# Kernel tuning notes

Measured on AMD Instinct MI355X. Metric: run time of the kernel, lower is better.

The kernel has to match this reference:

```python
import jax, jax.numpy as jnp
import numpy as np
import math

V, D, H, NL, L, B = 32000, 1024, 16, 6, 1024, 2
HD = D // H
EPS = 1e-5


def _positional(L, D):
    # matches torch: exp(arange(0,D,2) * -(log(1000)/D))
    div = jnp.exp(jnp.arange(0, D, 2, dtype=jnp.float32) * (-math.log(1000.0) / D))
    k = jnp.arange(L, dtype=jnp.float32)[:, None]
    pos = jnp.zeros((L, D), dtype=jnp.float32)
    pos = pos.at[:, 0::2].set(jnp.sin(k * div))
    pos = pos.at[:, 1::2].set(jnp.cos(k * div))
    return pos[None]  # [1, L, D]


def setup_inputs() -> dict:
    key = jax.random.key(0)
    ks = jax.random.split(key, 12)
    s = 0.02
    tokens = jax.random.randint(ks[0], (B, L), 0, V)
    emb = jax.random.normal(ks[1], (V, D), jnp.float32) * s
    pos = _positional(L, D)
    ln1_g = jnp.ones((NL, D), jnp.float32)
    ln1_b = jnp.zeros((NL, D), jnp.float32)
    ln2_g = jnp.ones((NL, D), jnp.float32)
    ln2_b = jnp.zeros((NL, D), jnp.float32)
    attn_w = jax.random.normal(ks[2], (NL, D, 3 * D), jnp.float32) * s
    attn_b = jnp.zeros((NL, 3 * D), jnp.float32)
    proj_w = jax.random.normal(ks[3], (NL, D, D), jnp.float32) * s
    proj_b = jnp.zeros((NL, D), jnp.float32)
    mlp_w1 = jax.random.normal(ks[4], (NL, D, 4 * D), jnp.float32) * s
    mlp_b1 = jnp.zeros((NL, 4 * D), jnp.float32)
    mlp_w2 = jax.random.normal(ks[5], (NL, 4 * D, D), jnp.float32) * s
    mlp_b2 = jnp.zeros((NL, D), jnp.float32)
    out_w = jax.random.normal(ks[6], (D, V), jnp.float32) * s
    return dict(tokens=tokens, pos=pos, emb=emb,
                ln1_g=ln1_g, ln1_b=ln1_b, ln2_g=ln2_g, ln2_b=ln2_b,
                attn_w=attn_w, attn_b=attn_b, proj_w=proj_w, proj_b=proj_b,
                mlp_w1=mlp_w1, mlp_b1=mlp_b1, mlp_w2=mlp_w2, mlp_b2=mlp_b2,
                out_w=out_w)


def _ln(x, g, b):
    mu = jnp.mean(x, -1, keepdims=True)
    var = jnp.mean(jnp.square(x - mu), -1, keepdims=True)
    return (x - mu) * jax.lax.rsqrt(var + EPS) * g + b


def _block(x, p, causal_mask):
    ln1_g, ln1_b, ln2_g, ln2_b, aw, ab, pw, pb, w1, b1, w2, b2 = p
    h = _ln(x, ln1_g, ln1_b)
    qkv = h @ aw + ab                      # [B, L, 3D]
    q, k, v = jnp.split(qkv, 3, axis=-1)
    Bc, Lc = x.shape[0], x.shape[1]
    q = q.reshape(Bc, Lc, H, HD)
    k = k.reshape(Bc, Lc, H, HD)
    v = v.reshape(Bc, Lc, H, HD)
    scores = jnp.einsum('blhd,bmhd->bhlm', q, k) * (1.0 / math.sqrt(HD))
    scores = jnp.where(causal_mask, scores, -jnp.inf)
    attn = jax.nn.softmax(scores, axis=-1)
    y = jnp.einsum('bhlm,bmhd->blhd', attn, v).reshape(Bc, Lc, D)
    x = x + (y @ pw + pb)
    r = _ln(x, ln2_g, ln2_b)
    # NOTE: original ModuleList order applies GELU AFTER the second linear
    r = jax.nn.gelu((r @ w1 + b1) @ w2 + b2, approximate=False)
    return x + r


def reference(tokens, pos, emb, ln1_g, ln1_b, ln2_g, ln2_b,
              attn_w, attn_b, proj_w, proj_b,
              mlp_w1, mlp_b1, mlp_w2, mlp_b2, out_w):
    x = emb[tokens] + pos                  # [B, L, D]
    Lc = x.shape[1]
    causal_mask = jnp.tril(jnp.ones((Lc, Lc), bool))[None, None]
    for i in range(NL):
        p = (ln1_g[i], ln1_b[i], ln2_g[i], ln2_b[i],
             attn_w[i], attn_b[i], proj_w[i], proj_b[i],
             mlp_w1[i], mlp_b1[i], mlp_w2[i], mlp_b2[i])
        x = _block(x, p, causal_mask)
    return x @ out_w                       # [B, L, V] logits
```

## Files before the change

kernel.cpp:

```cpp
#include <hip/hip_runtime.h>
#include <hip/hip_bf16.h>
#include <math.h>

typedef __bf16 bf16;
typedef __bf16 bf16x4 __attribute__((ext_vector_type(4)));
typedef __bf16 bf16x8 __attribute__((ext_vector_type(8)));
typedef float f32x4 __attribute__((ext_vector_type(4)));

__device__ __forceinline__ void gld_lds16(const void* g, void* l) {
    __builtin_amdgcn_global_load_lds(
        (const __attribute__((address_space(1))) unsigned int*)g,
        (__attribute__((address_space(3))) unsigned int*)l, 16, 0, 0);
}

#define VMW(n) asm volatile("s_waitcnt vmcnt(" #n ")" ::: "memory")
#define BARR() asm volatile("s_barrier" ::: "memory")

__global__ __launch_bounds__(256) void k_embed(const int* __restrict__ tok,
                                               const float* __restrict__ emb,
                                               const float* __restrict__ pos,
                                               float* __restrict__ x) {
    int row = blockIdx.x;
    int l = row & 1023;
    int tk = tok[row];
    const float4* e = (const float4*)(emb + (size_t)tk * 1024);
    const float4* p = (const float4*)(pos + (size_t)l * 1024);
    float4* o = (float4*)(x + (size_t)row * 1024);
    float4 a = e[threadIdx.x], b = p[threadIdx.x];
    o[threadIdx.x] = make_float4(a.x + b.x, a.y + b.y, a.z + b.z, a.w + b.w);
}

__global__ __launch_bounds__(256) void k_ln(const float* __restrict__ x,
                                            const float* __restrict__ g,
                                            const float* __restrict__ b,
                                            bf16* __restrict__ out) {
    int row = blockIdx.x;
    int t = threadIdx.x;
    const float4* xr = (const float4*)(x + (size_t)row * 1024);
    float4 v = xr[t];
    float s1 = v.x + v.y + v.z + v.w;
    float s2 = v.x * v.x + v.y * v.y + v.z * v.z + v.w * v.w;
#pragma unroll
    for (int o = 32; o; o >>= 1) { s1 += __shfl_down(s1, o); s2 += __shfl_down(s2, o); }
    __shared__ float ps1[4], ps2[4], stat[2];
    int lane = t & 63, wid = t >> 6;
    if (lane == 0) { ps1[wid] = s1; ps2[wid] = s2; }
    __syncthreads();
    if (t == 0) {
        float a1 = ps1[0] + ps1[1] + ps1[2] + ps1[3];
        float a2 = ps2[0] + ps2[1] + ps2[2] + ps2[3];
        float mu = a1 * (1.f / 1024.f);
        float var = a2 * (1.f / 1024.f) - mu * mu;
        stat[0] = mu; stat[1] = rsqrtf(var + 1e-5f);
    }
    __syncthreads();
    float mu = stat[0], rs = stat[1];
    const float4* gv = (const float4*)g;
    const float4* bv = (const float4*)b;
    float4 gg = gv[t], bb = bv[t];
    bf16x4 o4;
    o4[0] = (bf16)((v.x - mu) * rs * gg.x + bb.x);
    o4[1] = (bf16)((v.y - mu) * rs * gg.y + bb.y);
    o4[2] = (bf16)((v.z - mu) * rs * gg.z + bb.z);
    o4[3] = (bf16)((v.w - mu) * rs * gg.w + bb.w);
    *(bf16x4*)(out + (size_t)row * 1024 + t * 4) = o4;
}

__global__ __launch_bounds__(256) void k_cast(const float* __restrict__ x, bf16* __restrict__ o) {
    int i = blockIdx.x * 256 + threadIdx.x;
    float4 v = ((const float4*)x)[i];
    bf16x4 b;
    b[0] = (bf16)v.x; b[1] = (bf16)v.y; b[2] = (bf16)v.z; b[3] = (bf16)v.w;
    ((bf16x4*)o)[i] = b;
}

__device__ __forceinline__ void transpose64(const float* __restrict__ W,
                                            bf16* __restrict__ WT,
                                            int K, int N, int n0, int k0, int t,
                                            float (*tile)[65]) {
    int tx = t & 15, ty = t >> 4;
#pragma unroll
    for (int i = 0; i < 64; i += 16) {
        float4 v = *(const float4*)&W[(size_t)(k0 + ty + i) * N + n0 + tx * 4];
        tile[ty + i][tx * 4 + 0] = v.x;
        tile[ty + i][tx * 4 + 1] = v.y;
        tile[ty + i][tx * 4 + 2] = v.z;
        tile[ty + i][tx * 4 + 3] = v.w;
    }
    __syncthreads();
    int n = t >> 3, ks = t & 7;
#pragma unroll
    for (int pass = 0; pass < 2; ++pass) {
        int nn = n + pass * 32;
        bf16x8 v;
#pragma unroll
        for (int j = 0; j < 8; ++j) v[j] = (bf16)tile[ks * 8 + j][nn];
        *(bf16x8*)&WT[(size_t)(n0 + nn) * K + k0 + ks * 8] = v;
    }
}

__global__ __launch_bounds__(256) void k_transpose_layer(const float* __restrict__ aw,
                                                         const float* __restrict__ pw,
                                                         const float* __restrict__ m1,
                                                         const float* __restrict__ m2,
                                                         bf16* __restrict__ wT) {
    __shared__ float tile[64][65];
    int bid = blockIdx.x;
    const float* src; bf16* dst; int K, N, tn, tk;
    if (bid < 768)       { src = aw; dst = wT;            K = 1024; N = 3072; tn = bid % 48; tk = bid / 48; }
    else if (bid < 1024) { int b = bid - 768;  src = pw; dst = wT + 3145728; K = 1024; N = 1024; tn = b % 16; tk = b / 16; }
    else if (bid < 2048) { int b = bid - 1024; src = m1; dst = wT + 4194304; K = 1024; N = 4096; tn = b % 64; tk = b / 64; }
    else                 { int b = bid - 2048; src = m2; dst = wT + 8388608; K = 4096; N = 1024; tn = b % 16; tk = b / 16; }
    transpose64(src, dst, K, N, tn * 64, tk * 64, threadIdx.x, tile);
}

__global__ __launch_bounds__(256) void k_transpose_out(const float* __restrict__ W,
                                                       bf16* __restrict__ WT) {
    __shared__ float tile[64][65];
    int bid = blockIdx.x;
    int tn = bid % 500, tk = bid / 500;
    transpose64(W, WT, 1024, 32000, tn * 64, tk * 64, threadIdx.x, tile);
}

__device__ __forceinline__ void stage128(const char* Ab, const char* Bb,
                                         char* As, char* Bs, int Kb, int k0b, int t) {
#pragma unroll
    for (int j = 0; j < 4; ++j) {
        int idx = j * 256 + t;
        int row = idx >> 3;
        int cb = (idx & 7) << 4;
        int scb = cb ^ ((row & 7) << 4);
        gld_lds16(Ab + (size_t)row * Kb + k0b + scb, As + idx * 16);
        gld_lds16(Bb + (size_t)row * Kb + k0b + scb, Bs + idx * 16);
    }
}

template <int EPI>
__global__ __launch_bounds__(256) void k_gemm2(const bf16* __restrict__ A,
                                               const bf16* __restrict__ BT,
                                               const float* __restrict__ bias,
                                               const float* __restrict__ resid,
                                               float* __restrict__ outf,
                                               bf16* __restrict__ outb,
                                               int N, int K) {
    __shared__ __align__(16) bf16 As[2][128 * 64];
    __shared__ __align__(16) bf16 Bs[2][128 * 64];
    int per = gridDim.x >> 3;
    int tile = (blockIdx.x & 7) * per + (blockIdx.x >> 3);
    int bm = tile & 15, bn = tile >> 4;
    int t = threadIdx.x, lane = t & 63;
    int wr = t >> 7, wc = (t >> 6) & 1;
    f32x4 acc[4][4] = {};
    const char* Ab = (const char*)(A + (size_t)bm * 128 * K);
    const char* Bb = (const char*)(BT + (size_t)bn * 128 * K);
    int Kb = K * 2;
    int nk = K >> 6;
    stage128(Ab, Bb, (char*)As[0], (char*)Bs[0], Kb, 0, t);
    VMW(0); BARR();
    for (int tt = 0; tt < nk; ++tt) {
        int cur = tt & 1;
        if (tt + 1 < nk)
            stage128(Ab, Bb, (char*)As[cur ^ 1], (char*)Bs[cur ^ 1], Kb, (tt + 1) * 128, t);
        const char* Ac = (const char*)As[cur];
        const char* Bc = (const char*)Bs[cur];
#pragma unroll
        for (int kk = 0; kk < 2; ++kk) {
            bf16x8 af[4], bfr[4];
            int cb = kk * 64 + ((lane >> 4) << 4);
#pragma unroll
            for (int m = 0; m < 4; ++m) {
                int r = wr * 64 + m * 16 + (lane & 15);
                af[m] = *(const bf16x8*)(Ac + r * 128 + (cb ^ ((r & 7) << 4)));
            }
#pragma unroll
            for (int n = 0; n < 4; ++n) {
                int r = wc * 64 + n * 16 + (lane & 15);
                bfr[n] = *(const bf16x8*)(Bc + r * 128 + (cb ^ ((r & 7) << 4)));
            }
#pragma unroll
            for (int m = 0; m < 4; ++m)
#pragma unroll
                for (int n = 0; n < 4; ++n)
                    acc[m][n] = __builtin_amdgcn_mfma_f32_16x16x32_bf16(af[m], bfr[n], acc[m][n], 0, 0, 0);
        }
        VMW(0); BARR();
    }
    int row0 = bm * 128 + wr * 64 + ((lane >> 4) << 2);
    int col0 = bn * 128 + wc * 64 + (lane & 15);
#pragma unroll
    for (int m = 0; m < 4; ++m) {
#pragma unroll
        for (int n = 0; n < 4; ++n) {
            int col = col0 + n * 16;
            float bv = bias[col];
#pragma unroll
            for (int r = 0; r < 4; ++r) {
                int row = row0 + m * 16 + r;
                size_t idx = (size_t)row * N + col;
                float v = acc[m][n][r] + bv;
                if (EPI == 0) {
                    outb[idx] = (bf16)v;
                } else if (EPI == 1) {
                    outf[idx] = resid[idx] + v;
                } else {
                    outf[idx] = resid[idx] + 0.5f * v * (1.0f + erff(v * 0.70710678118f));
                }
            }
        }
    }
}

__device__ __forceinline__ void stage64(const char* Ab, const char* Bb,
                                        char* As, char* Bs, int Kb, int k0b, int t) {
#pragma unroll
    for (int j = 0; j < 2; ++j) {
        int idx = j * 256 + t;
        int row = idx >> 3;
        int cb = (idx & 7) << 4;
        int scb = cb ^ ((row & 7) << 4);
        gld_lds16(Ab + (size_t)row * Kb + k0b + scb, As + idx * 16);
        gld_lds16(Bb + (size_t)row * Kb + k0b + scb, Bs + idx * 16);
    }
}

template <int EPI>
__global__ __launch_bounds__(256) void k_gemm64(const bf16* __restrict__ A,
                                                const bf16* __restrict__ BT,
                                                const float* __restrict__ bias,
                                                const float* __restrict__ resid,
                                                float* __restrict__ outf,
                                                int N, int K) {
    __shared__ __align__(16) bf16 As[2][64 * 64];
    __shared__ __align__(16) bf16 Bs[2][64 * 64];
    int per = gridDim.x >> 3;
    int tile = (blockIdx.x & 7) * per + (blockIdx.x >> 3);
    int bm = tile & 31, bn = tile >> 5;
    int t = threadIdx.x, lane = t & 63, wid = t >> 6;
    f32x4 acc[4] = {};
    const char* Ab = (const char*)(A + (size_t)bm * 64 * K);
    const char* Bb = (const char*)(BT + (size_t)bn * 64 * K);
    int Kb = K * 2;
    int nk = K >> 6;
    stage64(Ab, Bb, (char*)As[0], (char*)Bs[0], Kb, 0, t);
    VMW(0); BARR();
    for (int tt = 0; tt < nk; ++tt) {
        int cur = tt & 1;
        if (tt + 1 < nk)
            stage64(Ab, Bb, (char*)As[cur ^ 1], (char*)Bs[cur ^ 1], Kb, (tt + 1) * 128, t);
        const char* Ac = (const char*)As[cur];
        const char* Bc = (const char*)Bs[cur];
#pragma unroll
        for (int kk = 0; kk < 2; ++kk) {
            int cb = kk * 64 + ((lane >> 4) << 4);
            int ra = wid * 16 + (lane & 15);
            bf16x8 af = *(const bf16x8*)(Ac + ra * 128 + (cb ^ ((ra & 7) << 4)));
            bf16x8 bfr[4];
#pragma unroll
            for (int n = 0; n < 4; ++n) {
                int r = n * 16 + (lane & 15);
                bfr[n] = *(const bf16x8*)(Bc + r * 128 + (cb ^ ((r & 7) << 4)));
            }
#pragma unroll
            for (int n = 0; n < 4; ++n)
                acc[n] = __builtin_amdgcn_mfma_f32_16x16x32_bf16(af, bfr[n], acc[n], 0, 0, 0);
        }
        VMW(0); BARR();
    }
    int row0 = bm * 64 + wid * 16 + ((lane >> 4) << 2);
    int col0 = bn * 64 + (lane & 15);
#pragma unroll
    for (int n = 0; n < 4; ++n) {
        int col = col0 + n * 16;
        float bv = bias[col];
#pragma unroll
        for (int r = 0; r < 4; ++r) {
            int row = row0 + r;
            size_t idx = (size_t)row * N + col;
            float v = acc[n][r] + bv;
            if (EPI == 1) {
                outf[idx] = resid[idx] + v;
            } else {
                outf[idx] = resid[idx] + 0.5f * v * (1.0f + erff(v * 0.70710678118f));
            }
        }
    }
}

__device__ __forceinline__ void stage_full256(const char* gtile, char* ldst,
                                              int Kb, int t) {
#pragma unroll
    for (int j = 0; j < 4; ++j) {
        int idx = j * 512 + t;
        int row = idx >> 3;
        int cb = (idx & 7) << 4;
        int scb = cb ^ ((row & 7) << 4);
        gld_lds16(gtile + (size_t)row * Kb + scb, ldst + idx * 16);
    }
}

__device__ __forceinline__ void stage_half256(const char* gtile, char* ldst,
                                              int Kb, int t, int half) {
#pragma unroll
    for (int j = 0; j < 2; ++j) {
        int idx = (half * 2 + j) * 512 + t;
        int row = idx >> 3;
        int cb = (idx & 7) << 4;
        int scb = cb ^ ((row & 7) << 4);
        gld_lds16(gtile + (size_t)row * Kb + scb, ldst + idx * 16);
    }
}

template <int MH, int NH>
__device__ __forceinline__ void phase_rd(const char* Ac, const char* Bc,
                                         int lrow, int lk, int wm, int wn,
                                         bf16x8 (&af)[4][2], bf16x8 (&bfr)[2][2]) {
#pragma unroll
    for (int kk = 0; kk < 2; ++kk) {
        int cb = kk * 64 + lk * 16;
#pragma unroll
        for (int m = 0; m < 4; ++m) {
            int row = (MH * 4 + m) * 32 + wm * 16 + lrow;
            af[m][kk] = *(const bf16x8*)(Ac + row * 128 + (cb ^ ((row & 7) << 4)));
        }
#pragma unroll
        for (int n = 0; n < 2; ++n) {
            int row = (NH * 2 + n) * 64 + wn * 16 + lrow;
            bfr[n][kk] = *(const bf16x8*)(Bc + row * 128 + (cb ^ ((row & 7) << 4)));
        }
    }
}

template <int MH, int NH>
__device__ __forceinline__ void phase_mm(bf16x8 (&af)[4][2], bf16x8 (&bfr)[2][2],
                                         f32x4 (&acc)[8][4]) {
    __builtin_amdgcn_s_setprio(1);
#pragma unroll
    for (int kk = 0; kk < 2; ++kk)
#pragma unroll
        for (int m = 0; m < 4; ++m)
#pragma unroll
            for (int n = 0; n < 2; ++n)
                acc[MH * 4 + m][NH * 2 + n] = __builtin_amdgcn_mfma_f32_16x16x32_bf16(
                    af[m][kk], bfr[n][kk], acc[MH * 4 + m][NH * 2 + n], 0, 0, 0);
    __builtin_amdgcn_s_setprio(0);
    __builtin_amdgcn_sched_barrier(0);
}

__global__ __launch_bounds__(512, 1) void k_gemm256(const bf16* __restrict__ A,
                                                    const bf16* __restrict__ BT,
                                                    float* __restrict__ outf,
                                                    int N, int K) {
    __shared__ __align__(16) bf16 Asb[2][256 * 64];
    __shared__ __align__(16) bf16 Bsb[3][256 * 64];
    int t = threadIdx.x, lane = t & 63, wid = t >> 6;
    int wm = wid >> 2, wn = wid & 3;
    int lrow = lane & 15, lk = lane >> 4;
    int tile = (blockIdx.x & 7) * 125 + (blockIdx.x >> 3);
    int bm = tile & 7;
    int bn = tile >> 3;

    const char* Ab = (const char*)(A + (size_t)bm * 256 * K);
    const char* Bb = (const char*)(BT + (size_t)bn * 256 * K);
    int Kb = K * 2;
    int nk = K >> 6;
    f32x4 acc[8][4] = {};

    stage_full256(Ab, (char*)Asb[0], Kb, t);
    stage_full256(Bb, (char*)Bsb[0], Kb, t);
    stage_full256(Bb + 128, (char*)Bsb[1], Kb, t);

    for (int tt = 0; tt < nk; ++tt) {
        int ka = (tt + 1 < nk) ? tt + 1 : nk - 1;
        int kb = (tt + 2 < nk) ? tt + 2 : nk - 1;
        const char* Ac = (const char*)Asb[tt & 1];
        const char* Bc = (const char*)Bsb[tt % 3];
        char* An = (char*)Asb[(tt + 1) & 1];
        char* Bn = (char*)Bsb[(tt + 2) % 3];
        const char* Ag = Ab + (size_t)ka * 128;
        const char* Bg = Bb + (size_t)kb * 128;
        VMW(4); BARR();
        bf16x8 af[4][2], bfr[2][2];
        phase_rd<0, 0>(Ac, Bc, lrow, lk, wm, wn, af, bfr);
        stage_half256(Ag, An, Kb, t, 0);
        BARR();
        phase_mm<0, 0>(af, bfr, acc);
        BARR();
        phase_rd<0, 1>(Ac, Bc, lrow, lk, wm, wn, af, bfr);
        stage_half256(Ag, An, Kb, t, 1);
        BARR();
        phase_mm<0, 1>(af, bfr, acc);
        BARR();
        phase_rd<1, 0>(Ac, Bc, lrow, lk, wm, wn, af, bfr);
        stage_half256(Bg, Bn, Kb, t, 0);
        BARR();
        phase_mm<1, 0>(af, bfr, acc);
        BARR();
        phase_rd<1, 1>(Ac, Bc, lrow, lk, wm, wn, af, bfr);
        stage_half256(Bg, Bn, Kb, t, 1);
        BARR();
        phase_mm<1, 1>(af, bfr, acc);
        BARR();
    }

    size_t row0 = (size_t)bm * 256 + wm * 16 + (lane >> 4) * 4;
    int col0 = bn * 256 + wn * 16 + (lane & 15);
#pragma unroll
    for (int mi = 0; mi < 8; ++mi) {
#pragma unroll
        for (int ni = 0; ni < 4; ++ni) {
            int col = col0 + ni * 64;
#pragma unroll
            for (int r = 0; r < 4; ++r) {
                size_t row = row0 + mi * 32 + r;
                outf[row * N + col] = acc[mi][ni][r];
            }
        }
    }
}

__global__ __launch_bounds__(256) void k_attn(const bf16* __restrict__ qkv, bf16* __restrict__ y) {
    int tile = (blockIdx.x & 7) * 64 + (blockIdx.x >> 3);
    int qb = tile & 15;
    int bh = tile >> 4;
    int b = bh >> 4, h = bh & 15;
    int t = threadIdx.x, lane = t & 63, wid = t >> 6;
    int lr = lane & 15, lk = lane >> 4;
    int tok0 = b << 10;
    int q0 = qb << 6;
    __shared__ __align__(16) bf16 Qs[64 * 64];
    __shared__ __align__(16) bf16 Ks[64 * 64];
    __shared__ __align__(16) bf16 Vt[64 * 64];
    __shared__ __align__(16) bf16 Ps[4 * 16 * 64];
    const char* qbase = (const char*)qkv;
#pragma unroll
    for (int j = 0; j < 2; ++j) {
        int off = (j * 256 + t) * 16;
        int row = off >> 7, colb = off & 127;
        int scb = colb ^ ((row & 7) << 4);
        gld_lds16(qbase + ((size_t)(tok0 + q0 + row) * 3072 + h * 64) * 2 + scb, (char*)Qs + off);
    }
    VMW(0);
    __syncthreads();
    int qrw = wid * 16 + lr;
    int qsw = (qrw & 7) << 4;
    bf16x8 aq0 = *(const bf16x8*)((const char*)Qs + qrw * 128 + ((lk * 16) ^ qsw));
    bf16x8 aq1 = *(const bf16x8*)((const char*)Qs + qrw * 128 + ((64 + lk * 16) ^ qsw));
    f32x4 o[4] = {};
    float mrun[4], lrun[4];
#pragma unroll
    for (int r = 0; r < 4; ++r) { mrun[r] = -INFINITY; lrun[r] = 0.f; }
    int qrow = q0 + wid * 16 + lk * 4;

    for (int kv0 = 0; kv0 <= q0; kv0 += 64) {
        __syncthreads();
#pragma unroll
        for (int j = 0; j < 2; ++j) {
            int off = (j * 256 + t) * 16;
            int row = off >> 7, colb = off & 127;
            int scb = colb ^ ((row & 7) << 4);
            gld_lds16(qbase + ((size_t)(tok0 + kv0 + row) * 3072 + 1024 + h * 64) * 2 + scb,
                      (char*)Ks + off);
        }
        {
            int kv = t >> 2, d0 = (t & 3) * 16;
            const bf16* vrow = qkv + (size_t)(tok0 + kv0 + kv) * 3072 + 2048 + h * 64 + d0;
#pragma unroll
            for (int e4 = 0; e4 < 4; ++e4) {
                bf16x4 vv = *(const bf16x4*)(vrow + e4 * 4);
#pragma unroll
                for (int i = 0; i < 4; ++i) {
                    int d = d0 + e4 * 4 + i;
                    Vt[d * 64 + (kv ^ ((d & 7) << 3))] = vv[i];
                }
            }
        }
        VMW(0);
        __syncthreads();
        f32x4 s[4];
#pragma unroll
        for (int n = 0; n < 4; ++n) {
            int krw = n * 16 + lr;
            int ksw = (krw & 7) << 4;
            const char* kb = (const char*)Ks + krw * 128;
            bf16x8 bk0 = *(const bf16x8*)(kb + ((lk * 16) ^ ksw));
            bf16x8 bk1 = *(const bf16x8*)(kb + ((64 + lk * 16) ^ ksw));
            f32x4 z = {};
            z = __builtin_amdgcn_mfma_f32_16x16x32_bf16(aq0, bk0, z, 0, 0, 0);
            z = __builtin_amdgcn_mfma_f32_16x16x32_bf16(aq1, bk1, z, 0, 0, 0);
            s[n] = z;
        }
        float mx[4];
#pragma unroll
        for (int r = 0; r < 4; ++r) mx[r] = -INFINITY;
#pragma unroll
        for (int n = 0; n < 4; ++n) {
            int col = kv0 + n * 16 + lr;
#pragma unroll
            for (int r = 0; r < 4; ++r) {
                float sv = s[n][r] * 0.125f;
                sv = (col <= qrow + r) ? sv : -INFINITY;
                s[n][r] = sv;
                mx[r] = fmaxf(mx[r], sv);
            }
        }
#pragma unroll
        for (int r = 0; r < 4; ++r)
#pragma unroll
            for (int m = 1; m < 16; m <<= 1) mx[r] = fmaxf(mx[r], __shfl_xor(mx[r], m));
        float scl[4];
#pragma unroll
        for (int r = 0; r < 4; ++r) {
            float mn = fmaxf(mrun[r], mx[r]);
            scl[r] = __expf(mrun[r] - mn);
            mrun[r] = mn;
        }
        float rs[4] = {0.f, 0.f, 0.f, 0.f};
#pragma unroll
        for (int n = 0; n < 4; ++n)
#pragma unroll
            for (int r = 0; r < 4; ++r) {
                float p = __expf(s[n][r] - mrun[r]);
                s[n][r] = p;
                rs[r] += p;
            }
#pragma unroll
        for (int r = 0; r < 4; ++r) {
#pragma unroll
            for (int m = 1; m < 16; m <<= 1) rs[r] += __shfl_xor(rs[r], m);
            lrun[r] = lrun[r] * scl[r] + rs[r];
        }
#pragma unroll
        for (int n = 0; n < 4; ++n)
#pragma unroll
            for (int r = 0; r < 4; ++r) {
                o[n][r] *= scl[r];
                int prow = lk * 4 + r;
                Ps[wid * 1024 + prow * 64 + ((n * 16 + lr) ^ ((prow & 7) << 3))] = (bf16)s[n][r];
            }
        int psw = (lr & 7) << 3;
        const bf16* pb = Ps + wid * 1024 + lr * 64;
        bf16x8 ap0 = *(const bf16x8*)(pb + ((lk * 8) ^ psw));
        bf16x8 ap1 = *(const bf16x8*)(pb + ((32 + lk * 8) ^ psw));
#pragma unroll
        for (int n = 0; n < 4; ++n) {
            int vrw = n * 16 + lr;
            int vsw = (vrw & 7) << 3;
            const bf16* vb = Vt + vrw * 64;
            bf16x8 bv0 = *(const bf16x8*)(vb + ((lk * 8) ^ vsw));
            bf16x8 bv1 = *(const bf16x8*)(vb + ((32 + lk * 8) ^ vsw));
            o[n] = __builtin_amdgcn_mfma_f32_16x16x32_bf16(ap0, bv0, o[n], 0, 0, 0);
            o[n] = __builtin_amdgcn_mfma_f32_16x16x32_bf16(ap1, bv1, o[n], 0, 0, 0);
        }
    }
#pragma unroll
    for (int n = 0; n < 4; ++n)
#pragma unroll
        for (int r = 0; r < 4; ++r) {
            int row = tok0 + qrow + r;
            y[(size_t)row * 1024 + h * 64 + n * 16 + lr] = (bf16)(o[n][r] / lrun[r]);
        }
}

extern "C" void kernel_launch(void* const* d_in, const int* in_sizes, int n_in,
                              void* d_out, int out_size, void* d_ws, size_t ws_size,
                              hipStream_t stream) {
    const int*   tokens = (const int*)d_in[0];
    const float* pos    = (const float*)d_in[1];
    const float* emb    = (const float*)d_in[2];
    const float* ln1_g  = (const float*)d_in[3];
    const float* ln1_b  = (const float*)d_in[4];
    const float* ln2_g  = (const float*)d_in[5];
    const float* ln2_b  = (const float*)d_in[6];
    const float* attn_w = (const float*)d_in[7];
    const float* attn_b = (const float*)d_in[8];
    const float* proj_w = (const float*)d_in[9];
    const float* proj_b = (const float*)d_in[10];
    const float* mlp_w1 = (const float*)d_in[11];
    const float* mlp_b1 = (const float*)d_in[12];
    const float* mlp_w2 = (const float*)d_in[13];
    const float* mlp_b2 = (const float*)d_in[14];
    const float* out_w  = (const float*)d_in[15];
    float* out = (float*)d_out;

    char* ws = (char*)d_ws;
    size_t off = 0;
    auto alloc = [&](size_t bytes) {
        void* p = ws + off;
        off = (off + bytes + 255) & ~(size_t)255;
        return p;
    };
    float* x   = (float*)alloc((size_t)2048 * 1024 * 4);
    bf16* hb   = (bf16*)alloc((size_t)2048 * 1024 * 2);
    bf16* qkvb = (bf16*)alloc((size_t)2048 * 3072 * 2);
    bf16* yb   = (bf16*)alloc((size_t)2048 * 1024 * 2);
    bf16* hidb = (bf16*)alloc((size_t)2048 * 4096 * 2);
    bf16* wT   = (bf16*)alloc((size_t)32000 * 1024 * 2);

    k_embed<<<2048, 256, 0, stream>>>(tokens, emb, pos, x);

    for (int i = 0; i < 6; ++i) {
        k_transpose_layer<<<3072, 256, 0, stream>>>(
            attn_w + (size_t)i * 1024 * 3072, proj_w + (size_t)i * 1024 * 1024,
            mlp_w1 + (size_t)i * 1024 * 4096, mlp_w2 + (size_t)i * 4096 * 1024, wT);
        k_ln<<<2048, 256, 0, stream>>>(x, ln1_g + i * 1024, ln1_b + i * 1024, hb);
        k_gemm2<0><<<384, 256, 0, stream>>>(hb, wT, attn_b + i * 3072,
                                            nullptr, nullptr, qkvb, 3072, 1024);
        k_attn<<<512, 256, 0, stream>>>(qkvb, yb);
        k_gemm64<1><<<512, 256, 0, stream>>>(yb, wT + 3145728, proj_b + i * 1024,
                                             x, x, 1024, 1024);
        k_ln<<<2048, 256, 0, stream>>>(x, ln2_g + i * 1024, ln2_b + i * 1024, hb);
        k_gemm2<0><<<512, 256, 0, stream>>>(hb, wT + 4194304, mlp_b1 + i * 4096,
                                            nullptr, nullptr, hidb, 4096, 1024);
        k_gemm64<2><<<512, 256, 0, stream>>>(hidb, wT + 8388608, mlp_b2 + i * 1024,
                                             x, x, 1024, 4096);
    }

    k_cast<<<2048, 256, 0, stream>>>(x, hb);
    k_transpose_out<<<8000, 256, 0, stream>>>(out_w, wT);
    k_gemm256<<<1000, 512, 0, stream>>>(hb, wT, out, 32000, 1024);
}
```

Before: 1.217 ms.

## Overlap next-layer weight transposes with attention and fuse final bf16 cast

```diff
diff --git a/kernel.cpp b/kernel.cpp
--- a/kernel.cpp
+++ b/kernel.cpp
@@ -66,14 +66,6 @@
     *(bf16x4*)(out + (size_t)row * 1024 + t * 4) = o4;
 }
 
-__global__ __launch_bounds__(256) void k_cast(const float* __restrict__ x, bf16* __restrict__ o) {
-    int i = blockIdx.x * 256 + threadIdx.x;
-    float4 v = ((const float4*)x)[i];
-    bf16x4 b;
-    b[0] = (bf16)v.x; b[1] = (bf16)v.y; b[2] = (bf16)v.z; b[3] = (bf16)v.w;
-    ((bf16x4*)o)[i] = b;
-}
-
 __device__ __forceinline__ void transpose64(const float* __restrict__ W,
                                             bf16* __restrict__ WT,
                                             int K, int N, int n0, int k0, int t,
@@ -99,27 +91,25 @@
     }
 }
 
+__device__ __forceinline__ void tr_layer_block(int bid,
+                                               const float* aw, const float* pw,
+                                               const float* m1, const float* m2,
+                                               bf16* wT, int t, float (*tile)[65]) {
+    const float* src; bf16* dst; int K, N, tn, tk;
+    if (bid < 768)       { src = aw; dst = wT;            K = 1024; N = 3072; tn = bid % 48; tk = bid / 48; }
+    else if (bid < 1024) { int b = bid - 768;  src = pw; dst = wT + 3145728; K = 1024; N = 1024; tn = b % 16; tk = b / 16; }
+    else if (bid < 2048) { int b = bid - 1024; src = m1; dst = wT + 4194304; K = 1024; N = 4096; tn = b % 64; tk = b / 64; }
+    else                 { int b = bid - 2048; src = m2; dst = wT + 8388608; K = 4096; N = 1024; tn = b % 16; tk = b / 16; }
+    transpose64(src, dst, K, N, tn * 64, tk * 64, t, tile);
+}
+
 __global__ __launch_bounds__(256) void k_transpose_layer(const float* __restrict__ aw,
                                                          const float* __restrict__ pw,
                                                          const float* __restrict__ m1,
                                                          const float* __restrict__ m2,
                                                          bf16* __restrict__ wT) {
     __shared__ float tile[64][65];
-    int bid = blockIdx.x;
-    const float* src; bf16* dst; int K, N, tn, tk;
-    if (bid < 768)       { src = aw; dst = wT;            K = 1024; N = 3072; tn = bid % 48; tk = bid / 48; }
-    else if (bid < 1024) { int b = bid - 768;  src = pw; dst = wT + 3145728; K = 1024; N = 1024; tn = b % 16; tk = b / 16; }
-    else if (bid < 2048) { int b = bid - 1024; src = m1; dst = wT + 4194304; K = 1024; N = 4096; tn = b % 64; tk = b / 64; }
-    else                 { int b = bid - 2048; src = m2; dst = wT + 8388608; K = 4096; N = 1024; tn = b % 16; tk = b / 16; }
-    transpose64(src, dst, K, N, tn * 64, tk * 64, threadIdx.x, tile);
-}
-
-__global__ __launch_bounds__(256) void k_transpose_out(const float* __restrict__ W,
-                                                       bf16* __restrict__ WT) {
-    __shared__ float tile[64][65];
-    int bid = blockIdx.x;
-    int tn = bid % 500, tk = bid / 500;
-    transpose64(W, WT, 1024, 32000, tn * 64, tk * 64, threadIdx.x, tile);
+    tr_layer_block(blockIdx.x, aw, pw, m1, m2, wT, threadIdx.x, tile);
 }
 
 __device__ __forceinline__ void stage128(const char* Ab, const char* Bb,
@@ -229,6 +219,7 @@
                                                 const float* __restrict__ bias,
                                                 const float* __restrict__ resid,
                                                 float* __restrict__ outf,
+                                                bf16* __restrict__ outb,
                                                 int N, int K) {
     __shared__ __align__(16) bf16 As[2][64 * 64];
     __shared__ __align__(16) bf16 Bs[2][64 * 64];
@@ -277,11 +268,14 @@
             int row = row0 + r;
             size_t idx = (size_t)row * N + col;
             float v = acc[n][r] + bv;
+            float res;
             if (EPI == 1) {
-                outf[idx] = resid[idx] + v;
+                res = resid[idx] + v;
             } else {
-                outf[idx] = resid[idx] + 0.5f * v * (1.0f + erff(v * 0.70710678118f));
-            }
+                res = resid[idx] + 0.5f * v * (1.0f + erff(v * 0.70710678118f));
+            }
+            outf[idx] = res;
+            if (outb) outb[idx] = (bf16)res;
         }
     }
 }
@@ -418,19 +412,41 @@
     }
 }
 
-__global__ __launch_bounds__(256) void k_attn(const bf16* __restrict__ qkv, bf16* __restrict__ y) {
-    int tile = (blockIdx.x & 7) * 64 + (blockIdx.x >> 3);
+__global__ __launch_bounds__(256) void k_attn_tr(const bf16* __restrict__ qkv,
+                                                 bf16* __restrict__ y,
+                                                 const float* __restrict__ aw,
+                                                 const float* __restrict__ pw,
+                                                 const float* __restrict__ m1,
+                                                 const float* __restrict__ m2,
+                                                 bf16* __restrict__ wTnext,
+                                                 const float* __restrict__ outw,
+                                                 bf16* __restrict__ outT) {
+    __shared__ __align__(16) char smem[32768];
+    int bidg = blockIdx.x;
+    int t = threadIdx.x;
+    if (bidg >= 512) {
+        int tb = bidg - 512;
+        float (*tile)[65] = (float(*)[65])smem;
+        if (aw) {
+            tr_layer_block(tb, aw, pw, m1, m2, wTnext, t, tile);
+        } else {
+            int tn = tb % 500, tk = tb / 500;
+            transpose64(outw, outT, 1024, 32000, tn * 64, tk * 64, t, tile);
+        }
+        return;
+    }
+    bf16* Qs = (bf16*)smem;
+    bf16* Ks = Qs + 4096;
+    bf16* Vt = Ks + 4096;
+    bf16* Ps = Vt + 4096;
+    int tile = (bidg & 7) * 64 + (bidg >> 3);
     int qb = tile & 15;
     int bh = tile >> 4;
     int b = bh >> 4, h = bh & 15;
-    int t = threadIdx.x, lane = t & 63, wid = t >> 6;
+    int lane = t & 63, wid = t >> 6;
     int lr = lane & 15, lk = lane >> 4;
     int tok0 = b << 10;
     int q0 = qb << 6;
-    __shared__ __align__(16) bf16 Qs[64 * 64];
-    __shared__ __align__(16) bf16 Ks[64 * 64];
-    __shared__ __align__(16) bf16 Vt[64 * 64];
-    __shared__ __align__(16) bf16 Ps[4 * 16 * 64];
     const char* qbase = (const char*)qkv;
 #pragma unroll
     for (int j = 0; j < 2; ++j) {
@@ -594,28 +610,36 @@
     bf16* qkvb = (bf16*)alloc((size_t)2048 * 3072 * 2);
     bf16* yb   = (bf16*)alloc((size_t)2048 * 1024 * 2);
     bf16* hidb = (bf16*)alloc((size_t)2048 * 4096 * 2);
-    bf16* wT   = (bf16*)alloc((size_t)32000 * 1024 * 2);
+    bf16* outT = (bf16*)alloc((size_t)32000 * 1024 * 2);
+    bf16* slot1 = (bf16*)alloc((size_t)9437184 * 2);
+    bf16* slots[2] = { outT, slot1 };
 
     k_embed<<<2048, 256, 0, stream>>>(tokens, emb, pos, x);
+    k_transpose_layer<<<3072, 256, 0, stream>>>(attn_w, proj_w, mlp_w1, mlp_w2, slots[0]);
 
     for (int i = 0; i < 6; ++i) {
-        k_transpose_layer<<<3072, 256, 0, stream>>>(
-            attn_w + (size_t)i * 1024 * 3072, proj_w + (size_t)i * 1024 * 1024,
-            mlp_w1 + (size_t)i * 1024 * 4096, mlp_w2 + (size_t)i * 4096 * 1024, wT);
+        bf16* wT = slots[i & 1];
         k_ln<<<2048, 256, 0, stream>>>(x, ln1_g + i * 1024, ln1_b + i * 1024, hb);
         k_gemm2<0><<<384, 256, 0, stream>>>(hb, wT, attn_b + i * 3072,
                                             nullptr, nullptr, qkvb, 3072, 1024);
-        k_attn<<<512, 256, 0, stream>>>(qkvb, yb);
+        if (i < 5) {
+            int j = i + 1;
+            k_attn_tr<<<3584, 256, 0, stream>>>(qkvb, yb,
+                attn_w + (size_t)j * 1024 * 3072, proj_w + (size_t)j * 1024 * 1024,
+                mlp_w1 + (size_t)j * 1024 * 4096, mlp_w2 + (size_t)j * 4096 * 1024,
+                slots[j & 1], nullptr, nullptr);
+        } else {
+            k_attn_tr<<<8512, 256, 0, stream>>>(qkvb, yb,
+                nullptr, nullptr, nullptr, nullptr, nullptr, out_w, outT);
+        }
         k_gemm64<1><<<512, 256, 0, stream>>>(yb, wT + 3145728, proj_b + i * 1024,
-                                             x, x, 1024, 1024);
+                                             x, x, nullptr, 1024, 1024);
         k_ln<<<2048, 256, 0, stream>>>(x, ln2_g + i * 1024, ln2_b + i * 1024, hb);
         k_gemm2<0><<<512, 256, 0, stream>>>(hb, wT + 4194304, mlp_b1 + i * 4096,
                                             nullptr, nullptr, hidb, 4096, 1024);
         k_gemm64<2><<<512, 256, 0, stream>>>(hidb, wT + 8388608, mlp_b2 + i * 1024,
-                                             x, x, 1024, 4096);
-    }
-
-    k_cast<<<2048, 256, 0, stream>>>(x, hb);
-    k_transpose_out<<<8000, 256, 0, stream>>>(out_w, wT);
-    k_gemm256<<<1000, 512, 0, stream>>>(hb, wT, out, 32000, 1024);
-}
+                                             x, x, (i == 5) ? hb : nullptr, 1024, 4096);
+    }
+
+    k_gemm256<<<1000, 512, 0, stream>>>(hb, outT, out, 32000, 1024);
+}
```

Result: faster. 1.137 ms (-6.6%).
